# Performance work log

Hardware: AMD Instinct MI355X
Metric: run time of the kernel (lower is better)

Reference implementation:

```python
import jax, jax.numpy as jnp
import numpy as np

VOCAB, EMB, HID, LABELS, SEQ = 30522, 768, 1024, 2, 4096


def setup_inputs() -> dict:
    key = jax.random.key(0)
    ks = jax.random.split(key, 8)
    s = 0.02  # keep gate pre-activations in a sane range
    return {
        "sentence": jax.random.randint(ks[0], (SEQ,), 0, VOCAB),
        "emb": jax.random.normal(ks[1], (VOCAB, EMB), jnp.float32),
        "w_ih": jax.random.normal(ks[2], (4 * HID, EMB), jnp.float32) * s,
        "w_hh": jax.random.normal(ks[3], (4 * HID, HID), jnp.float32) * s,
        "b_ih": jax.random.normal(ks[4], (4 * HID,), jnp.float32) * s,
        "b_hh": jax.random.normal(ks[5], (4 * HID,), jnp.float32) * s,
        "w_out": jax.random.normal(ks[6], (LABELS, HID), jnp.float32) * s,
        "b_out": jax.random.normal(ks[7], (LABELS,), jnp.float32) * s,
    }


def reference(sentence, emb, w_ih, w_hh, b_ih, b_hh, w_out, b_out):
    H = w_hh.shape[1]
    x = emb[sentence]                       # [T, E] frozen embedding lookup
    xg = x @ w_ih.T + (b_ih + b_hh)         # [T, 4H] precompute input-to-gate GEMM

    def cell(carry, xgt):
        h, c = carry
        gates = xgt + w_hh @ h              # [4H]
        i, f, g, o = jnp.split(gates, 4)
        i = jax.nn.sigmoid(i)
        f = jax.nn.sigmoid(f)
        g = jnp.tanh(g)
        o = jax.nn.sigmoid(o)
        c = f * c + i * g
        h = o * jnp.tanh(c)
        return (h, c), None

    h0 = jnp.zeros((H,), x.dtype)
    c0 = jnp.zeros((H,), x.dtype)
    (h_T, _), _ = jax.lax.scan(cell, (h0, c0), xg)
    y = h_T @ w_out.T + b_out               # [label_size]
    return jax.nn.log_softmax(y[None, :], axis=-1)  # [1, label_size]
```

## Files before the change

kernel.cpp:

```cpp
#include <hip/hip_runtime.h>
#include <hip/hip_bf16.h>

#define VOCAB 30522
#define EMB   768
#define HID   1024
#define SEQ   4096
#define NG    4096
#define NWG   64
#define RT    512

static __device__ __forceinline__ unsigned short f32_to_bf16(float f) {
  unsigned u = __float_as_uint(f);
  u = (u + 0x7fffu + ((u >> 16) & 1u)) >> 16;
  return (unsigned short)u;
}

#define BM 64
#define BN 64
#define BK 16

__global__ __launch_bounds__(256) void xg_gemm(
    const int* __restrict__ sent, const float* __restrict__ emb,
    const float* __restrict__ w_ih, const float* __restrict__ b_ih,
    const float* __restrict__ b_hh, __hip_bfloat16* __restrict__ xg) {
  __shared__ float As[BK][BM + 4];
  __shared__ float Bs[BK][BN + 4];
  const int tid = threadIdx.x;
  const int n0 = blockIdx.x * BN;
  const int m0 = blockIdx.y * BM;
  const int tx = tid & 15, ty = tid >> 4;
  const int lr = tid >> 2;
  const int lk = (tid & 3) * 4;

  const int arow = sent[m0 + lr];
  const float* aptr = emb + (size_t)arow * EMB + lk;
  const float* bptr = w_ih + (size_t)(n0 + lr) * EMB + lk;

  float acc[4][4] = {};

  for (int k0 = 0; k0 < EMB; k0 += BK) {
    float4 av = *(const float4*)(aptr + k0);
    float4 bv = *(const float4*)(bptr + k0);
    __syncthreads();
    As[lk + 0][lr] = av.x; As[lk + 1][lr] = av.y;
    As[lk + 2][lr] = av.z; As[lk + 3][lr] = av.w;
    Bs[lk + 0][lr] = bv.x; Bs[lk + 1][lr] = bv.y;
    Bs[lk + 2][lr] = bv.z; Bs[lk + 3][lr] = bv.w;
    __syncthreads();
#pragma unroll
    for (int k = 0; k < BK; ++k) {
      float4 a = *(const float4*)&As[k][ty * 4];
      float4 b = *(const float4*)&Bs[k][tx * 4];
      acc[0][0] = fmaf(a.x, b.x, acc[0][0]); acc[0][1] = fmaf(a.x, b.y, acc[0][1]);
      acc[0][2] = fmaf(a.x, b.z, acc[0][2]); acc[0][3] = fmaf(a.x, b.w, acc[0][3]);
      acc[1][0] = fmaf(a.y, b.x, acc[1][0]); acc[1][1] = fmaf(a.y, b.y, acc[1][1]);
      acc[1][2] = fmaf(a.y, b.z, acc[1][2]); acc[1][3] = fmaf(a.y, b.w, acc[1][3]);
      acc[2][0] = fmaf(a.z, b.x, acc[2][0]); acc[2][1] = fmaf(a.z, b.y, acc[2][1]);
      acc[2][2] = fmaf(a.z, b.z, acc[2][2]); acc[2][3] = fmaf(a.z, b.w, acc[2][3]);
      acc[3][0] = fmaf(a.w, b.x, acc[3][0]); acc[3][1] = fmaf(a.w, b.y, acc[3][1]);
      acc[3][2] = fmaf(a.w, b.z, acc[3][2]); acc[3][3] = fmaf(a.w, b.w, acc[3][3]);
    }
  }

#pragma unroll
  for (int i = 0; i < 4; ++i) {
    int gm = m0 + ty * 4 + i;
#pragma unroll
    for (int j = 0; j < 4; ++j) {
      int gn = n0 + tx * 4 + j;
      float v = acc[i][j] + b_ih[gn] + b_hh[gn];
      xg[(size_t)gm * NG + gn] = __float2bfloat16(v);
    }
  }
}

__global__ __launch_bounds__(RT, 1) void lstm_rec(
    const float* __restrict__ w_hh, const __hip_bfloat16* __restrict__ xg,
    unsigned long long* __restrict__ slots) {
  __shared__ unsigned hl[2][512];

  const int tid  = threadIdx.x;
  const int wg   = blockIdx.x;
  const int lane = tid & 63;
  const int wv   = tid >> 6;
  const int c    = lane;

  unsigned wp[8][8];
#pragma unroll
  for (int s = 0; s < 8; ++s) {
    const int q = s >> 1, m = s & 1;
    const int gr = q * HID + wg * 16 + 2 * wv + m;
    const float* wr = w_hh + (size_t)gr * HID;
#pragma unroll
    for (int k = 0; k < 8; ++k) {
      float2 wv2 = *(const float2*)(wr + 2 * (c + 64 * k));
      wp[s][k] = ((unsigned)f32_to_bf16(wv2.y) << 16) | (unsigned)f32_to_bf16(wv2.x);
    }
  }
#pragma unroll
  for (int s = 0; s < 8; ++s)
#pragma unroll
    for (int k = 0; k < 8; ++k)
      asm volatile("" : "+v"(wp[s][k]));

  float cst = 0.f;
  const int m = lane & 1;

  for (int t = 0; t < SEQ; ++t) {
    float xqv = 0.f;
    if (lane < 8) {
      const int q = lane >> 1;
      xqv = __bfloat162float(
          xg[(size_t)t * NG + q * HID + wg * 16 + 2 * wv + (lane & 1)]);
    }

    const unsigned long long want = (unsigned long long)t;
    unsigned long long* sp = slots + ((t & 1) << 9) + tid;
    unsigned long long va = __hip_atomic_load(sp, __ATOMIC_RELAXED, __HIP_MEMORY_SCOPE_AGENT);
    unsigned long long vb = __hip_atomic_load(sp, __ATOMIC_RELAXED, __HIP_MEMORY_SCOPE_AGENT);
    unsigned long long v;
    for (;;) {
      if ((va >> 32) == want) { v = va; break; }
      va = __hip_atomic_load(sp, __ATOMIC_RELAXED, __HIP_MEMORY_SCOPE_AGENT);
      if ((vb >> 32) == want) { v = vb; break; }
      vb = __hip_atomic_load(sp, __ATOMIC_RELAXED, __HIP_MEMORY_SCOPE_AGENT);
    }
    hl[t & 1][tid] = (unsigned)v;
    __syncthreads();

    const unsigned* hb = hl[t & 1];
    float hx[8], hy[8];
#pragma unroll
    for (int k = 0; k < 8; ++k) {
      unsigned hw = hb[c + 64 * k];
      hx[k] = __uint_as_float(hw << 16);
      hy[k] = __uint_as_float(hw & 0xffff0000u);
    }

    float acc[8];
#pragma unroll
    for (int s = 0; s < 8; ++s) {
      float a = 0.f;
#pragma unroll
      for (int k = 0; k < 8; ++k) {
        unsigned w = wp[s][k];
        a = fmaf(__uint_as_float(w << 16),          hx[k], a);
        a = fmaf(__uint_as_float(w & 0xffff0000u),  hy[k], a);
      }
      acc[s] = a;
    }

#pragma unroll
    for (int M = 1, n = 8; M <= 4; M <<= 1, n >>= 1) {
#pragma unroll
      for (int j = 0; j < 4; ++j) {
        if (j < (n >> 1)) {
          float u  = (lane & M) ? acc[2 * j + 1] : acc[2 * j];
          float u2 = (lane & M) ? acc[2 * j]     : acc[2 * j + 1];
          acc[j] = u + __shfl_xor(u2, M, 64);
        }
      }
    }
    float r = acc[0];
    r += __shfl_xor(r, 8, 64);
    r += __shfl_xor(r, 16, 64);
    r += __shfl_xor(r, 32, 64);

    {
      const int s = lane & 7;
      const bool isg = (s >> 1) == 2;
      float z = r + xqv;
      z = isg ? 2.f * z : z;
      float sg = 1.f / (1.f + __expf(-z));
      r = isg ? fmaf(2.f, sg, -1.f) : sg;
    }

    float i_ = __shfl(r, m,     64);
    float f_ = __shfl(r, 2 + m, 64);
    float g_ = __shfl(r, 4 + m, 64);
    float o_ = __shfl(r, 6 + m, 64);

    cst = fmaf(f_, cst, i_ * g_);
    float th = fmaf(2.f, 1.f / (1.f + __expf(-2.f * cst)), -1.f);
    float hn = o_ * th;

    float hn1 = __shfl(hn, 1, 64);
    if (lane == 0) {
      unsigned payload = ((unsigned)f32_to_bf16(hn1) << 16) | (unsigned)f32_to_bf16(hn);
      unsigned long long pv =
          ((unsigned long long)(unsigned)(t + 1) << 32) | (unsigned long long)payload;
      __hip_atomic_store(slots + (((t + 1) & 1) << 9) + (wg * 8 + wv), pv,
                         __ATOMIC_RELAXED, __HIP_MEMORY_SCOPE_AGENT);
    }
  }
}

__global__ __launch_bounds__(256) void head_kernel(
    const unsigned long long* __restrict__ hslots, const float* __restrict__ w_out,
    const float* __restrict__ b_out, float* __restrict__ out) {
  __shared__ float s0[256], s1[256];
  const int tid = threadIdx.x;
  float p0 = 0.f, p1 = 0.f;
  for (int w = tid; w < 512; w += 256) {
    unsigned pw = (unsigned)hslots[w];
    float h0 = __uint_as_float(pw << 16);
    float h1 = __uint_as_float(pw & 0xffff0000u);
    p0 = fmaf(h0, w_out[2 * w], fmaf(h1, w_out[2 * w + 1], p0));
    p1 = fmaf(h0, w_out[HID + 2 * w], fmaf(h1, w_out[HID + 2 * w + 1], p1));
  }
  s0[tid] = p0; s1[tid] = p1;
  __syncthreads();
  for (int off = 128; off; off >>= 1) {
    if (tid < off) { s0[tid] += s0[tid + off]; s1[tid] += s1[tid + off]; }
    __syncthreads();
  }
  if (tid == 0) {
    float y0 = s0[0] + b_out[0], y1 = s1[0] + b_out[1];
    float mx = fmaxf(y0, y1);
    float lse = mx + logf(expf(y0 - mx) + expf(y1 - mx));
    out[0] = y0 - lse;
    out[1] = y1 - lse;
  }
}

extern "C" void kernel_launch(void* const* d_in, const int* in_sizes, int n_in,
                              void* d_out, int out_size, void* d_ws, size_t ws_size,
                              hipStream_t stream) {
  const int*   sent  = (const int*)d_in[0];
  const float* emb   = (const float*)d_in[1];
  const float* w_ih  = (const float*)d_in[2];
  const float* w_hh  = (const float*)d_in[3];
  const float* b_ih  = (const float*)d_in[4];
  const float* b_hh  = (const float*)d_in[5];
  const float* w_out = (const float*)d_in[6];
  const float* b_out = (const float*)d_in[7];
  float* out = (float*)d_out;

  unsigned long long* slots = (unsigned long long*)d_ws;
  __hip_bfloat16* xg = (__hip_bfloat16*)((char*)d_ws + 16384);

  hipMemsetAsync(d_ws, 0, 16384, stream);

  dim3 ggrid(NG / BN, SEQ / BM);
  xg_gemm<<<ggrid, 256, 0, stream>>>(sent, emb, w_ih, b_ih, b_hh, xg);

  lstm_rec<<<NWG, RT, 0, stream>>>(w_hh, xg, slots);

  head_kernel<<<1, 256, 0, stream>>>(slots, w_out, b_out, out);
}
```

Baseline: 7.579 ms.

## Spread recurrence over 128 workgroups with fp32 register-resident recurrent weights

Doubles the number of workgroups in the persistent LSTM recurrence and halves threads per group, so each wave still owns 8 gate rows while each workgroup owns 8 hidden units instead of 16. With half the rows per CU, the recurrent weights are kept in registers as full fp32 instead of packed bf16, which removes the per-step unpacking shifts and masks and raises precision. Each thread now polls two handoff slots per step, and the cross-workgroup barrier involves twice as many participants. That may raise synchronisation latency, and the doubled register footprint may limit occupancy.

```diff
diff --git a/kernel.cpp b/kernel.cpp
--- a/kernel.cpp
+++ b/kernel.cpp
@@ -6,8 +6,8 @@
 #define HID   1024
 #define SEQ   4096
 #define NG    4096
-#define NWG   64
-#define RT    512
+#define NWG   128
+#define RT    256
 
 static __device__ __forceinline__ unsigned short f32_to_bf16(float f) {
   unsigned u = __float_as_uint(f);
@@ -84,48 +84,47 @@
   const int lane = tid & 63;
   const int wv   = tid >> 6;
   const int c    = lane;
-
-  unsigned wp[8][8];
+  const int m    = lane & 1;
+
+  unsigned wu[8][16];
 #pragma unroll
   for (int s = 0; s < 8; ++s) {
-    const int q = s >> 1, m = s & 1;
-    const int gr = q * HID + wg * 16 + 2 * wv + m;
+    const int q = s >> 1, mm = s & 1;
+    const int gr = q * HID + wg * 8 + 2 * wv + mm;
     const float* wr = w_hh + (size_t)gr * HID;
 #pragma unroll
     for (int k = 0; k < 8; ++k) {
       float2 wv2 = *(const float2*)(wr + 2 * (c + 64 * k));
-      wp[s][k] = ((unsigned)f32_to_bf16(wv2.y) << 16) | (unsigned)f32_to_bf16(wv2.x);
+      wu[s][2 * k]     = __float_as_uint(wv2.x);
+      wu[s][2 * k + 1] = __float_as_uint(wv2.y);
     }
   }
 #pragma unroll
   for (int s = 0; s < 8; ++s)
 #pragma unroll
-    for (int k = 0; k < 8; ++k)
-      asm volatile("" : "+v"(wp[s][k]));
+    for (int k = 0; k < 16; ++k)
+      asm volatile("" : "+v"(wu[s][k]));
 
   float cst = 0.f;
-  const int m = lane & 1;
 
   for (int t = 0; t < SEQ; ++t) {
     float xqv = 0.f;
     if (lane < 8) {
       const int q = lane >> 1;
       xqv = __bfloat162float(
-          xg[(size_t)t * NG + q * HID + wg * 16 + 2 * wv + (lane & 1)]);
+          xg[(size_t)t * NG + q * HID + wg * 8 + 2 * wv + (lane & 1)]);
     }
 
     const unsigned long long want = (unsigned long long)t;
-    unsigned long long* sp = slots + ((t & 1) << 9) + tid;
-    unsigned long long va = __hip_atomic_load(sp, __ATOMIC_RELAXED, __HIP_MEMORY_SCOPE_AGENT);
-    unsigned long long vb = __hip_atomic_load(sp, __ATOMIC_RELAXED, __HIP_MEMORY_SCOPE_AGENT);
-    unsigned long long v;
+    unsigned long long* sp = slots + ((t & 1) << 9) + 2 * tid;
+    unsigned long long v0, v1;
     for (;;) {
-      if ((va >> 32) == want) { v = va; break; }
-      va = __hip_atomic_load(sp, __ATOMIC_RELAXED, __HIP_MEMORY_SCOPE_AGENT);
-      if ((vb >> 32) == want) { v = vb; break; }
-      vb = __hip_atomic_load(sp, __ATOMIC_RELAXED, __HIP_MEMORY_SCOPE_AGENT);
-    }
-    hl[t & 1][tid] = (unsigned)v;
+      v0 = __hip_atomic_load(sp,     __ATOMIC_RELAXED, __HIP_MEMORY_SCOPE_AGENT);
+      v1 = __hip_atomic_load(sp + 1, __ATOMIC_RELAXED, __HIP_MEMORY_SCOPE_AGENT);
+      if (((v0 >> 32) == want) & ((v1 >> 32) == want)) break;
+    }
+    hl[t & 1][2 * tid]     = (unsigned)v0;
+    hl[t & 1][2 * tid + 1] = (unsigned)v1;
     __syncthreads();
 
     const unsigned* hb = hl[t & 1];
@@ -143,9 +142,8 @@
       float a = 0.f;
 #pragma unroll
       for (int k = 0; k < 8; ++k) {
-        unsigned w = wp[s][k];
-        a = fmaf(__uint_as_float(w << 16),          hx[k], a);
-        a = fmaf(__uint_as_float(w & 0xffff0000u),  hy[k], a);
+        a = fmaf(__uint_as_float(wu[s][2 * k]),     hx[k], a);
+        a = fmaf(__uint_as_float(wu[s][2 * k + 1]), hy[k], a);
       }
       acc[s] = a;
     }
@@ -189,7 +187,7 @@
       unsigned payload = ((unsigned)f32_to_bf16(hn1) << 16) | (unsigned)f32_to_bf16(hn);
       unsigned long long pv =
           ((unsigned long long)(unsigned)(t + 1) << 32) | (unsigned long long)payload;
-      __hip_atomic_store(slots + (((t + 1) & 1) << 9) + (wg * 8 + wv), pv,
+      __hip_atomic_store(slots + (((t + 1) & 1) << 9) + (wg * 4 + wv), pv,
                          __ATOMIC_RELAXED, __HIP_MEMORY_SCOPE_AGENT);
     }
   }
```

Result: no change. 7.480 ms (-1.3%).
